# Optimization experiments

Hardware: AMD Instinct MI355X
Metric: run time of the kernel (lower is better)

The kernel has to match this reference:

```python
import jax, jax.numpy as jnp
import numpy as np

B, T, C, H = 2, 64, 384, 768
LR, MOM, DECAY = 0.01, 0.9, 0.001


def pscan(gates, tokens):
    """parallel_scan_log: x[t] = gates[t]*x[t-1] + tokens[t] along axis 1.
    gates [B,S], tokens [B,S,...]."""
    extra = tokens.ndim - gates.ndim
    g = gates.reshape(gates.shape + (1,) * extra)
    g = jnp.clip(g, 1e-7, 1.0 - 1e-7)
    lc = jnp.cumsum(jnp.log(g), axis=1)              # log cumulative gates
    return jnp.exp(lc) * jnp.cumsum(tokens * jnp.exp(-lc), axis=1)


def setup_inputs():
    key = jax.random.key(0)
    ks = jax.random.split(key, 12)
    s = 0.02
    W0 = jax.random.normal(ks[0], (H, C), jnp.float32) * s
    W1 = jax.random.normal(ks[1], (C, H), jnp.float32) * s
    return {
        "x": jax.random.normal(ks[2], (B, T, C), jnp.float32),
        "Wq": jax.random.normal(ks[3], (C, C), jnp.float32) * s, "bq": jnp.zeros((C,), jnp.float32),
        "Wk": jax.random.normal(ks[4], (C, C), jnp.float32) * s, "bk": jnp.zeros((C,), jnp.float32),
        "Wv": jax.random.normal(ks[5], (C, C), jnp.float32) * s, "bv": jnp.zeros((C,), jnp.float32),
        "Wo": jax.random.normal(ks[6], (C, C), jnp.float32) * s, "bo": jnp.zeros((C,), jnp.float32),
        "init_query": jax.random.normal(ks[7], (1, 1, C), jnp.float32) * s,
        "sW0": jnp.broadcast_to(W0, (B, H, C)) + 0.0,
        "sb0": jnp.zeros((B, H), jnp.float32),
        "sW1": jnp.broadcast_to(W1, (B, C, H)) + 0.0,
        "sb1": jnp.zeros((B, C), jnp.float32),
    }


def reference(x, Wq, bq, Wk, bk, Wv, bv, Wo, bo, init_query, sW0, sb0, sW1, sb1):
    dt = x.dtype
    # ---- retrieval (causal: uses init_query since no previous segment) ----
    q = jnp.broadcast_to(init_query, (B, 1, C)) @ Wq.T + bq          # [B,1,C]
    h_pre = jnp.einsum('bqc,bhc->bqh', q, sW0) + sb0[:, None]
    h = h_pre * jax.nn.sigmoid(h_pre)                                 # SiLU
    pred = jnp.einsum('bqh,bch->bqc', h, sW1) + sb1[:, None]
    out = pred @ Wo.T + bo                                            # [B,1,C]

    # ---- test-time memory update: per-token MSE gradients ----
    k = x @ Wk.T + bk                                                 # [B,T,C]
    v = x @ Wv.T + bv
    h1_pre = jnp.einsum('btc,bhc->bth', k, sW0) + sb0[:, None]
    sig = jax.nn.sigmoid(h1_pre)
    h1 = h1_pre * sig
    p = jnp.einsum('bth,bch->btc', h1, sW1) + sb1[:, None]
    dp = p - v                                                        # d(MSE)/d(pred)
    dW1 = jnp.einsum('btc,bth->btch', dp, h1)                         # [B,T,C,H]
    db1 = dp
    dh1 = jnp.einsum('btc,bch->bth', dp, sW1)
    dh1p = dh1 * (sig * (1 + h1_pre * (1 - sig)))                     # SiLU grad
    dW0 = jnp.einsum('bth,btc->bthc', dh1p, k)                        # [B,T,H,C]
    db0 = dh1p

    # ---- momentum scan + decayed weight scan ----
    def update(W, g):
        surprise = -LR * g                                            # [B,T,...]
        m = pscan(jnp.full((B, T), MOM, dt), (1.0 - MOM) * surprise)  # EMA of surprises
        toks = jnp.concatenate([W[:, None], m], axis=1)               # seed with current weight
        gts = jnp.concatenate([jnp.ones((B, 1), dt),
                               jnp.full((B, T), 1.0 - DECAY, dt)], axis=1)
        return pscan(gts, toks)[:, -1]                                # final weight after segment

    nW0 = update(sW0, dW0)
    nb0 = update(sb0, db0)
    nW1 = update(sW1, dW1)
    nb1 = update(sb1, db1)
    return out, nW0, nb0, nW1, nb1
```

## Files before the change

kernel.cpp:

```cpp
#include <hip/hip_runtime.h>
#include <hip/hip_bf16.h>
#include <cmath>

#define BB 2
#define TT 64
#define CC 384
#define HH 768

#define O_OUT 0
#define O_NW0 768
#define O_NB0 (768 + 589824)
#define O_NW1 (O_NB0 + 1536)
#define O_NB1 (O_NW1 + 589824)

struct Coefs { float ct[TT]; float dfac; };

typedef __attribute__((ext_vector_type(8))) short bf16x8;
typedef __attribute__((ext_vector_type(4))) float f32x4;

__device__ __forceinline__ float bf2f(unsigned short u) {
    union { unsigned int i; float f; } x; x.i = ((unsigned int)u) << 16; return x.f;
}
__device__ __forceinline__ unsigned short f2bf(float f) {
    union { float f; unsigned int i; } u; u.f = f;
    unsigned int x = u.i;
    unsigned int r = (x + 0x7fffu + ((x >> 16) & 1u)) >> 16;
    return (unsigned short)r;
}
__device__ __forceinline__ f32x4 mfma16(bf16x8 a, bf16x8 b, f32x4 c) {
    return __builtin_amdgcn_mfma_f32_16x16x32_bf16(a, b, c, 0, 0, 0);
}
__device__ __forceinline__ bf16x8 ldbf8(const unsigned short* p) {
    return *(const bf16x8*)p;
}
__device__ __forceinline__ bf16x8 ldcvt8(const float* p) {
    float4 a = *(const float4*)p, b = *(const float4*)(p + 4);
    bf16x8 r;
    r[0] = (short)f2bf(a.x); r[1] = (short)f2bf(a.y); r[2] = (short)f2bf(a.z); r[3] = (short)f2bf(a.w);
    r[4] = (short)f2bf(b.x); r[5] = (short)f2bf(b.y); r[6] = (short)f2bf(b.z); r[7] = (short)f2bf(b.w);
    return r;
}
__device__ __forceinline__ bf16x8 ldcvt8s(const float* p, int stride) {
    bf16x8 r;
    #pragma unroll
    for (int i = 0; i < 8; ++i) r[i] = (short)f2bf(p[(size_t)i * stride]);
    return r;
}

__global__ void __launch_bounds__(256) k_qkv(
        const float* __restrict__ x,
        const float* __restrict__ Wk, const float* __restrict__ bk,
        const float* __restrict__ Wv, const float* __restrict__ bv,
        const float* __restrict__ Wq, const float* __restrict__ bq,
        const float* __restrict__ iq,
        unsigned short* __restrict__ kb_bf, float* __restrict__ vb,
        float* __restrict__ qb) {
    const int blk = blockIdx.x, j = threadIdx.x;
    const int wid = j >> 6, L = j & 63;
    const int w = blk * 4 + wid;
    const int lrow = L & 15, kq = (L >> 4) * 8, quad = L >> 4;
    int mf, npair;
    if (w < 192) { mf = w % 8; npair = w / 8; }
    else         { mf = 8;     npair = 24 + (w - 192); }
    const float* Arow = (mf < 8) ? (x + (size_t)(mf * 16 + lrow) * CC) : iq;
    const int n0 = npair * 32 + lrow, n1 = n0 + 16;
    const float* B0 = (n0 < CC) ? (Wk + (size_t)n0 * CC)
                    : (n0 < 2 * CC) ? (Wv + (size_t)(n0 - CC) * CC)
                    : (Wq + (size_t)(n0 - 2 * CC) * CC);
    const float* B1 = (n1 < CC) ? (Wk + (size_t)n1 * CC)
                    : (n1 < 2 * CC) ? (Wv + (size_t)(n1 - CC) * CC)
                    : (Wq + (size_t)(n1 - 2 * CC) * CC);
    f32x4 acc0 = {0,0,0,0}, acc1 = {0,0,0,0};
    #pragma unroll 2
    for (int s = 0; s < CC / 32; ++s) {
        int k = s * 32 + kq;
        bf16x8 a = ldcvt8(Arow + k);
        bf16x8 b0 = ldcvt8(B0 + k), b1 = ldcvt8(B1 + k);
        acc0 = mfma16(a, b0, acc0); acc1 = mfma16(a, b1, acc1);
    }
    #pragma unroll
    for (int ni = 0; ni < 2; ++ni) {
        f32x4 acc = ni == 0 ? acc0 : acc1;
        int n = npair * 32 + ni * 16 + lrow;
        if (mf < 8) {
            #pragma unroll
            for (int r = 0; r < 4; ++r) {
                int m = mf * 16 + quad * 4 + r;
                float v = acc[r];
                if (n < CC) kb_bf[(size_t)m * CC + n] = f2bf(v + bk[n]);
                else        vb[(size_t)m * CC + (n - CC)] = v + bv[n - CC];
            }
        } else if (quad == 0) {
            qb[n - 2 * CC] = acc[0] + bq[n - 2 * CC];
        }
    }
}

__global__ void __launch_bounds__(256) k_h1(
        const unsigned short* __restrict__ kb_bf, const float* __restrict__ qb,
        const float* __restrict__ sW0, const float* __restrict__ sb0,
        unsigned short* __restrict__ h1_bf, float* __restrict__ dsil,
        float* __restrict__ hret) {
    const int blk = blockIdx.x, j = threadIdx.x;
    const int b = blk / 30;
    const int wid = j >> 6, L = j & 63;
    const int w = (blk % 30) * 4 + wid;
    const int mf = w % 5, npair = w / 5;
    const int lrow = L & 15, kq = (L >> 4) * 8, quad = L >> 4;
    const unsigned short* Abf = kb_bf + (size_t)(b * TT + mf * 16 + lrow) * CC;
    const int n0 = npair * 32 + lrow;
    const float* B0 = sW0 + (size_t)(b * HH + n0) * CC;
    const float* B1 = B0 + 16 * CC;
    f32x4 acc0 = {0,0,0,0}, acc1 = {0,0,0,0};
    if (mf < 4) {
        #pragma unroll 2
        for (int s = 0; s < CC / 32; ++s) {
            int k = s * 32 + kq;
            bf16x8 a = ldbf8(Abf + k);
            bf16x8 b0 = ldcvt8(B0 + k), b1 = ldcvt8(B1 + k);
            acc0 = mfma16(a, b0, acc0); acc1 = mfma16(a, b1, acc1);
        }
    } else {
        #pragma unroll 2
        for (int s = 0; s < CC / 32; ++s) {
            int k = s * 32 + kq;
            bf16x8 a = ldcvt8(qb + k);
            bf16x8 b0 = ldcvt8(B0 + k), b1 = ldcvt8(B1 + k);
            acc0 = mfma16(a, b0, acc0); acc1 = mfma16(a, b1, acc1);
        }
    }
    #pragma unroll
    for (int ni = 0; ni < 2; ++ni) {
        f32x4 acc = ni == 0 ? acc0 : acc1;
        int n = npair * 32 + ni * 16 + lrow;
        float bias = sb0[b * HH + n];
        if (mf < 4) {
            #pragma unroll
            for (int r = 0; r < 4; ++r) {
                int t = mf * 16 + quad * 4 + r;
                float pre = acc[r] + bias;
                float sig = 1.f / (1.f + expf(-pre));
                size_t idx = (size_t)(b * TT + t) * HH + n;
                h1_bf[idx] = f2bf(pre * sig);
                dsil[idx]  = sig * (1.f + pre * (1.f - sig));
            }
        } else if (quad == 0) {
            float pre = acc[0] + bias;
            float sig = 1.f / (1.f + expf(-pre));
            hret[b * HH + n] = pre * sig;
        }
    }
}

__global__ void __launch_bounds__(256) k_p(
        const unsigned short* __restrict__ h1_bf, const float* __restrict__ hret,
        const float* __restrict__ vb,
        const float* __restrict__ sW1, const float* __restrict__ sb1,
        unsigned short* __restrict__ dp_bf, float* __restrict__ pred) {
    const int blk = blockIdx.x, j = threadIdx.x;
    const int b = blk / 15;
    const int wid = j >> 6, L = j & 63;
    const int w = (blk % 15) * 4 + wid;
    const int mf = w % 5, npair = w / 5;
    const int lrow = L & 15, kq = (L >> 4) * 8, quad = L >> 4;
    const unsigned short* Abf = h1_bf + (size_t)(b * TT + mf * 16 + lrow) * HH;
    const float* Aq = hret + (size_t)b * HH;
    const int n0 = npair * 32 + lrow;
    const float* B0 = sW1 + (size_t)(b * CC + n0) * HH;
    const float* B1 = B0 + 16 * HH;
    f32x4 acc0 = {0,0,0,0}, acc1 = {0,0,0,0};
    if (mf < 4) {
        #pragma unroll 2
        for (int s = 0; s < HH / 32; ++s) {
            int k = s * 32 + kq;
            bf16x8 a = ldbf8(Abf + k);
            bf16x8 b0 = ldcvt8(B0 + k), b1 = ldcvt8(B1 + k);
            acc0 = mfma16(a, b0, acc0); acc1 = mfma16(a, b1, acc1);
        }
    } else {
        #pragma unroll 2
        for (int s = 0; s < HH / 32; ++s) {
            int k = s * 32 + kq;
            bf16x8 a = ldcvt8(Aq + k);
            bf16x8 b0 = ldcvt8(B0 + k), b1 = ldcvt8(B1 + k);
            acc0 = mfma16(a, b0, acc0); acc1 = mfma16(a, b1, acc1);
        }
    }
    #pragma unroll
    for (int ni = 0; ni < 2; ++ni) {
        f32x4 acc = ni == 0 ? acc0 : acc1;
        int n = npair * 32 + ni * 16 + lrow;
        float bias = sb1[b * CC + n];
        if (mf < 4) {
            #pragma unroll
            for (int r = 0; r < 4; ++r) {
                int t = mf * 16 + quad * 4 + r;
                size_t idx = (size_t)(b * TT + t) * CC + n;
                dp_bf[idx] = f2bf(acc[r] + bias - vb[idx]);
            }
        } else if (quad == 0) {
            pred[b * CC + n] = acc[0] + bias;
        }
    }
}

__global__ void __launch_bounds__(256) k_epi1(
        const unsigned short* __restrict__ dp_bf,
        const unsigned short* __restrict__ h1_bf,
        const float* __restrict__ dsil,
        const float* __restrict__ sW1, const float* __restrict__ sb1,
        const float* __restrict__ pred,
        const float* __restrict__ Wo, const float* __restrict__ bo,
        unsigned short* __restrict__ dh1p_bf,
        float* __restrict__ out, Coefs cf) {
    __shared__ float smem[6144];
    const int blk = blockIdx.x, j = threadIdx.x;
    if (blk < 48) {
        const int b = blk / 24;
        const int wid = j >> 6, L = j & 63;
        const int w = (blk % 24) * 4 + wid;
        const int mf = w % 4, npair = w / 4;
        const int lrow = L & 15, kq = (L >> 4) * 8, quad = L >> 4;
        const unsigned short* Abf = dp_bf + (size_t)(b * TT + mf * 16 + lrow) * CC;
        const int n0 = npair * 32 + lrow, n1 = n0 + 16;
        const float* Bb = sW1 + (size_t)b * CC * HH;
        f32x4 acc0 = {0,0,0,0}, acc1 = {0,0,0,0};
        for (int s = 0; s < CC / 32; ++s) {
            int k = s * 32 + kq;
            bf16x8 a = ldbf8(Abf + k);
            bf16x8 b0 = ldcvt8s(Bb + (size_t)k * HH + n0, HH);
            bf16x8 b1 = ldcvt8s(Bb + (size_t)k * HH + n1, HH);
            acc0 = mfma16(a, b0, acc0); acc1 = mfma16(a, b1, acc1);
        }
        #pragma unroll
        for (int ni = 0; ni < 2; ++ni) {
            f32x4 acc = ni == 0 ? acc0 : acc1;
            int n = npair * 32 + ni * 16 + lrow;
            #pragma unroll
            for (int r = 0; r < 4; ++r) {
                int t = mf * 16 + quad * 4 + r;
                size_t idx = (size_t)(b * TT + t) * HH + n;
                dh1p_bf[idx] = f2bf(acc[r] * dsil[idx]);
            }
        }
    } else if (blk < 336) {
        float* a_t = smem;
        float* e_t = smem + 2048;
        const int u = blk - 48;
        const int b = u / 144, rem = u % 144;
        const int c0 = (rem / 12) * 32, h0 = (rem % 12) * 64;
        for (int i = j; i < TT * 32; i += 256) {
            int t = i >> 5, c = i & 31;
            a_t[t * 32 + c] = cf.ct[t] * bf2f(dp_bf[((size_t)(b * TT + t)) * CC + c0 + c]);
        }
        for (int i = j; i < TT * 64; i += 256) {
            int t = i >> 6, h = i & 63;
            e_t[t * 64 + h] = bf2f(h1_bf[((size_t)(b * TT + t)) * HH + h0 + h]);
        }
        __syncthreads();
        const int ci = j & 31, hb = (j >> 5) * 8;
        float acc[8] = {0, 0, 0, 0, 0, 0, 0, 0};
        for (int t = 0; t < TT; ++t) {
            float av = a_t[t * 32 + ci];
            #pragma unroll
            for (int m = 0; m < 8; ++m) acc[m] += av * e_t[t * 64 + hb + m];
        }
        const size_t idx = ((size_t)b * CC + c0 + ci) * HH + h0 + hb;
        const float4* w4 = (const float4*)(sW1 + idx);
        float4 wa = w4[0], wb = w4[1];
        float4 o0, o1;
        o0.x = cf.dfac * wa.x - acc[0]; o0.y = cf.dfac * wa.y - acc[1];
        o0.z = cf.dfac * wa.z - acc[2]; o0.w = cf.dfac * wa.w - acc[3];
        o1.x = cf.dfac * wb.x - acc[4]; o1.y = cf.dfac * wb.y - acc[5];
        o1.z = cf.dfac * wb.z - acc[6]; o1.w = cf.dfac * wb.w - acc[7];
        *(float4*)(out + O_NW1 + idx) = o0;
        *(float4*)(out + O_NW1 + idx + 4) = o1;
        if (h0 == 0 && j < 32) {
            float s = 0.f;
            for (int t = 0; t < TT; ++t) s += a_t[t * 32 + j];
            out[O_NB1 + b * CC + c0 + j] = cf.dfac * sb1[b * CC + c0 + j] - s;
        }
    } else {
        const int rb = blk - 336;
        const int b = rb / 24, nt = rb % 24;
        if (j < CC / 4) ((float4*)smem)[j] = ((const float4*)(pred + b * CC))[j];
        __syncthreads();
        const int nl = j & 15, ks = j >> 4;
        const int n = nt * 16 + nl;
        const float4* wr = (const float4*)(Wo + (size_t)n * CC + ks * 24);
        float s = 0.f;
        #pragma unroll
        for (int i = 0; i < 6; ++i) {
            float4 a = wr[i];
            const float* v = smem + ks * 24 + i * 4;
            s += a.x * v[0] + a.y * v[1] + a.z * v[2] + a.w * v[3];
        }
        smem[1024 + ks * 17 + nl] = s;
        __syncthreads();
        if (j < 16) {
            int n2 = nt * 16 + j;
            float acc = bo[n2];
            #pragma unroll
            for (int kk = 0; kk < 16; ++kk) acc += smem[1024 + kk * 17 + j];
            out[O_OUT + b * CC + n2] = acc;
        }
    }
}

__global__ void __launch_bounds__(256) k_epi2(
        const unsigned short* __restrict__ dh1p_bf,
        const unsigned short* __restrict__ kb_bf,
        const float* __restrict__ sW0, const float* __restrict__ sb0,
        float* __restrict__ out, Coefs cf) {
    __shared__ float smem[6144];
    float* a_t = smem;
    float* e_t = smem + 2048;
    const int blk = blockIdx.x, j = threadIdx.x;
    const int b = blk / 144, rem = blk % 144;
    const int h0 = (rem / 6) * 32, c0 = (rem % 6) * 64;
    for (int i = j; i < TT * 32; i += 256) {
        int t = i >> 5, h = i & 31;
        a_t[t * 32 + h] = cf.ct[t] * bf2f(dh1p_bf[((size_t)(b * TT + t)) * HH + h0 + h]);
    }
    for (int i = j; i < TT * 64; i += 256) {
        int t = i >> 6, c = i & 63;
        e_t[t * 64 + c] = bf2f(kb_bf[((size_t)(b * TT + t)) * CC + c0 + c]);
    }
    __syncthreads();
    const int hi = j & 31, cb = (j >> 5) * 8;
    float acc[8] = {0, 0, 0, 0, 0, 0, 0, 0};
    for (int t = 0; t < TT; ++t) {
        float av = a_t[t * 32 + hi];
        #pragma unroll
        for (int m = 0; m < 8; ++m) acc[m] += av * e_t[t * 64 + cb + m];
    }
    const size_t idx = ((size_t)b * HH + h0 + hi) * CC + c0 + cb;
    const float4* w4 = (const float4*)(sW0 + idx);
    float4 wa = w4[0], wb = w4[1];
    float4 o0, o1;
    o0.x = cf.dfac * wa.x - acc[0]; o0.y = cf.dfac * wa.y - acc[1];
    o0.z = cf.dfac * wa.z - acc[2]; o0.w = cf.dfac * wa.w - acc[3];
    o1.x = cf.dfac * wb.x - acc[4]; o1.y = cf.dfac * wb.y - acc[5];
    o1.z = cf.dfac * wb.z - acc[6]; o1.w = cf.dfac * wb.w - acc[7];
    *(float4*)(out + O_NW0 + idx) = o0;
    *(float4*)(out + O_NW0 + idx + 4) = o1;
    if (c0 == 0 && j < 32) {
        float s = 0.f;
        for (int t = 0; t < TT; ++t) s += a_t[t * 32 + j];
        out[O_NB0 + b * HH + h0 + j] = cf.dfac * sb0[b * HH + h0 + j] - s;
    }
}

extern "C" void kernel_launch(void* const* d_in, const int* in_sizes, int n_in,
                              void* d_out, int out_size, void* d_ws, size_t ws_size,
                              hipStream_t stream) {
    const float* x   = (const float*)d_in[0];
    const float* Wq  = (const float*)d_in[1];
    const float* bq  = (const float*)d_in[2];
    const float* Wk  = (const float*)d_in[3];
    const float* bk  = (const float*)d_in[4];
    const float* Wv  = (const float*)d_in[5];
    const float* bv  = (const float*)d_in[6];
    const float* Wo  = (const float*)d_in[7];
    const float* bo  = (const float*)d_in[8];
    const float* iq  = (const float*)d_in[9];
    const float* sW0 = (const float*)d_in[10];
    const float* sb0 = (const float*)d_in[11];
    const float* sW1 = (const float*)d_in[12];
    const float* sb1 = (const float*)d_in[13];

    float* fw = (float*)d_ws;
    float* qb   = fw;
    float* hret = qb + 384;
    float* pred = hret + 1536;
    float* vb   = pred + 768;
    float* dsil = vb + 49152;
    unsigned short* us = (unsigned short*)(dsil + 98304);
    unsigned short* kb_bf   = us;
    unsigned short* h1_bf   = kb_bf + 49152;
    unsigned short* dp_bf   = h1_bf + 98304;
    unsigned short* dh1p_bf = dp_bf + 49152;

    Coefs cf;
    const double mom = 0.9, decay = 1.0 - 0.001, lr = 0.01;
    for (int s = 0; s < TT; ++s) {
        double sum = 0.0;
        for (int t = s; t < TT; ++t) sum += pow(decay, (double)(TT - 1 - t)) * pow(mom, (double)(t - s));
        cf.ct[s] = (float)(lr * (1.0 - mom) * sum);
    }
    cf.dfac = (float)pow(decay, (double)TT);

    k_qkv <<<dim3(51),  dim3(256), 0, stream>>>(x, Wk, bk, Wv, bv, Wq, bq, iq, kb_bf, vb, qb);
    k_h1  <<<dim3(60),  dim3(256), 0, stream>>>(kb_bf, qb, sW0, sb0, h1_bf, dsil, hret);
    k_p   <<<dim3(30),  dim3(256), 0, stream>>>(h1_bf, hret, vb, sW1, sb1, dp_bf, pred);
    k_epi1<<<dim3(384), dim3(256), 0, stream>>>(dp_bf, h1_bf, dsil, sW1, sb1, pred, Wo, bo,
                                                dh1p_bf, (float*)d_out, cf);
    k_epi2<<<dim3(288), dim3(256), 0, stream>>>(dh1p_bf, kb_bf, sW0, sb0, (float*)d_out, cf);
}
```

Baseline: 142.0 us.

## Fuse dh1 GEMM into dW0 epilogue and prefetch weights into cache in qkv

Drops the separate k_epi1 dh1 GEMM and k_epi2 launch. Each dW0 block now recomputes its 32-column dh1p slice directly into shared memory with MFMA, which removes the dh1p_bf round trip and one kernel launch at the cost of recomputing the sW1 GEMM across six c0 tiles. It also adds 512 extra blocks to k_qkv that read sW0, sW1 and Wo and write dummy sums, so these weights are warm in L2/MALL for later kernels. The warming is cache priming that adds memory traffic in the first kernel and relies on cache residency.

After: 138.2 us. 2.7% less time.

```diff
diff --git a/kernel.cpp b/kernel.cpp
--- a/kernel.cpp
+++ b/kernel.cpp
@@ -53,9 +53,25 @@
         const float* __restrict__ Wv, const float* __restrict__ bv,
         const float* __restrict__ Wq, const float* __restrict__ bq,
         const float* __restrict__ iq,
+        const float* __restrict__ sW0, const float* __restrict__ sW1,
+        const float* __restrict__ Wo,
         unsigned short* __restrict__ kb_bf, float* __restrict__ vb,
-        float* __restrict__ qb) {
+        float* __restrict__ qb, float* __restrict__ warm_sink) {
     const int blk = blockIdx.x, j = threadIdx.x;
+    if (blk >= 51) {
+        int t = (blk - 51) * 256 + j;
+        float acc = 0.f;
+        for (int g = t; g < 184320; g += 512 * 256) {
+            const float4* src; int off;
+            if      (g < 73728)  { src = (const float4*)sW0; off = g; }
+            else if (g < 147456) { src = (const float4*)sW1; off = g - 73728; }
+            else                 { src = (const float4*)Wo;  off = g - 147456; }
+            float4 v = src[off];
+            acc += v.x + v.y + v.z + v.w;
+        }
+        warm_sink[t] = acc;
+        return;
+    }
     const int wid = j >> 6, L = j & 63;
     const int w = blk * 4 + wid;
     const int lrow = L & 15, kq = (L >> 4) * 8, quad = L >> 4;
@@ -204,50 +220,22 @@
     }
 }
 
-__global__ void __launch_bounds__(256) k_epi1(
+__global__ void __launch_bounds__(256) k_epi(
         const unsigned short* __restrict__ dp_bf,
         const unsigned short* __restrict__ h1_bf,
+        const unsigned short* __restrict__ kb_bf,
         const float* __restrict__ dsil,
+        const float* __restrict__ sW0, const float* __restrict__ sb0,
         const float* __restrict__ sW1, const float* __restrict__ sb1,
         const float* __restrict__ pred,
         const float* __restrict__ Wo, const float* __restrict__ bo,
-        unsigned short* __restrict__ dh1p_bf,
         float* __restrict__ out, Coefs cf) {
     __shared__ float smem[6144];
     const int blk = blockIdx.x, j = threadIdx.x;
-    if (blk < 48) {
-        const int b = blk / 24;
-        const int wid = j >> 6, L = j & 63;
-        const int w = (blk % 24) * 4 + wid;
-        const int mf = w % 4, npair = w / 4;
-        const int lrow = L & 15, kq = (L >> 4) * 8, quad = L >> 4;
-        const unsigned short* Abf = dp_bf + (size_t)(b * TT + mf * 16 + lrow) * CC;
-        const int n0 = npair * 32 + lrow, n1 = n0 + 16;
-        const float* Bb = sW1 + (size_t)b * CC * HH;
-        f32x4 acc0 = {0,0,0,0}, acc1 = {0,0,0,0};
-        for (int s = 0; s < CC / 32; ++s) {
-            int k = s * 32 + kq;
-            bf16x8 a = ldbf8(Abf + k);
-            bf16x8 b0 = ldcvt8s(Bb + (size_t)k * HH + n0, HH);
-            bf16x8 b1 = ldcvt8s(Bb + (size_t)k * HH + n1, HH);
-            acc0 = mfma16(a, b0, acc0); acc1 = mfma16(a, b1, acc1);
-        }
-        #pragma unroll
-        for (int ni = 0; ni < 2; ++ni) {
-            f32x4 acc = ni == 0 ? acc0 : acc1;
-            int n = npair * 32 + ni * 16 + lrow;
-            #pragma unroll
-            for (int r = 0; r < 4; ++r) {
-                int t = mf * 16 + quad * 4 + r;
-                size_t idx = (size_t)(b * TT + t) * HH + n;
-                dh1p_bf[idx] = f2bf(acc[r] * dsil[idx]);
-            }
-        }
-    } else if (blk < 336) {
+    if (blk < 288) {
         float* a_t = smem;
         float* e_t = smem + 2048;
-        const int u = blk - 48;
-        const int b = u / 144, rem = u % 144;
+        const int b = blk / 144, rem = blk % 144;
         const int c0 = (rem / 12) * 32, h0 = (rem % 12) * 64;
         for (int i = j; i < TT * 32; i += 256) {
             int t = i >> 5, c = i & 31;
@@ -280,8 +268,65 @@
             for (int t = 0; t < TT; ++t) s += a_t[t * 32 + j];
             out[O_NB1 + b * CC + c0 + j] = cf.dfac * sb1[b * CC + c0 + j] - s;
         }
+    } else if (blk < 576) {
+        float* a_t = smem;
+        float* e_t = smem + 2048;
+        const int u = blk - 288;
+        const int b = u / 144, rem = u % 144;
+        const int h0 = (rem / 6) * 32, c0 = (rem % 6) * 64;
+        for (int i = j; i < TT * 64; i += 256) {
+            int t = i >> 6, c = i & 63;
+            e_t[t * 64 + c] = bf2f(kb_bf[((size_t)(b * TT + t)) * CC + c0 + c]);
+        }
+        const int wid = j >> 6, L = j & 63;
+        const int lrow = L & 15, kq = (L >> 4) * 8, quad = L >> 4;
+        const unsigned short* Abf = dp_bf + (size_t)(b * TT + wid * 16 + lrow) * CC;
+        const float* Bb = sW1 + (size_t)b * CC * HH;
+        const int n0 = h0 + lrow, n1 = h0 + 16 + lrow;
+        f32x4 acc0 = {0,0,0,0}, acc1 = {0,0,0,0};
+        for (int s = 0; s < CC / 32; ++s) {
+            int k = s * 32 + kq;
+            bf16x8 a = ldbf8(Abf + k);
+            bf16x8 b0 = ldcvt8s(Bb + (size_t)k * HH + n0, HH);
+            bf16x8 b1 = ldcvt8s(Bb + (size_t)k * HH + n1, HH);
+            acc0 = mfma16(a, b0, acc0); acc1 = mfma16(a, b1, acc1);
+        }
+        #pragma unroll
+        for (int ni = 0; ni < 2; ++ni) {
+            f32x4 acc = ni == 0 ? acc0 : acc1;
+            int hl = ni * 16 + lrow;
+            #pragma unroll
+            for (int r = 0; r < 4; ++r) {
+                int t = wid * 16 + quad * 4 + r;
+                float ds = dsil[(size_t)(b * TT + t) * HH + h0 + hl];
+                a_t[t * 32 + hl] = cf.ct[t] * (acc[r] * ds);
+            }
+        }
+        __syncthreads();
+        const int hi = j & 31, cb = (j >> 5) * 8;
+        float acc[8] = {0, 0, 0, 0, 0, 0, 0, 0};
+        for (int t = 0; t < TT; ++t) {
+            float av = a_t[t * 32 + hi];
+            #pragma unroll
+            for (int m = 0; m < 8; ++m) acc[m] += av * e_t[t * 64 + cb + m];
+        }
+        const size_t idx = ((size_t)b * HH + h0 + hi) * CC + c0 + cb;
+        const float4* w4 = (const float4*)(sW0 + idx);
+        float4 wa = w4[0], wb = w4[1];
+        float4 o0, o1;
+        o0.x = cf.dfac * wa.x - acc[0]; o0.y = cf.dfac * wa.y - acc[1];
+        o0.z = cf.dfac * wa.z - acc[2]; o0.w = cf.dfac * wa.w - acc[3];
+        o1.x = cf.dfac * wb.x - acc[4]; o1.y = cf.dfac * wb.y - acc[5];
+        o1.z = cf.dfac * wb.z - acc[6]; o1.w = cf.dfac * wb.w - acc[7];
+        *(float4*)(out + O_NW0 + idx) = o0;
+        *(float4*)(out + O_NW0 + idx + 4) = o1;
+        if (c0 == 0 && j < 32) {
+            float s = 0.f;
+            for (int t = 0; t < TT; ++t) s += a_t[t * 32 + j];
+            out[O_NB0 + b * HH + h0 + j] = cf.dfac * sb0[b * HH + h0 + j] - s;
+        }
     } else {
-        const int rb = blk - 336;
+        const int rb = blk - 576;
         const int b = rb / 24, nt = rb % 24;
         if (j < CC / 4) ((float4*)smem)[j] = ((const float4*)(pred + b * CC))[j];
         __syncthreads();
@@ -304,50 +349,6 @@
             for (int kk = 0; kk < 16; ++kk) acc += smem[1024 + kk * 17 + j];
             out[O_OUT + b * CC + n2] = acc;
         }
-    }
-}
-
-__global__ void __launch_bounds__(256) k_epi2(
-        const unsigned short* __restrict__ dh1p_bf,
-        const unsigned short* __restrict__ kb_bf,
-        const float* __restrict__ sW0, const float* __restrict__ sb0,
-        float* __restrict__ out, Coefs cf) {
-    __shared__ float smem[6144];
-    float* a_t = smem;
-    float* e_t = smem + 2048;
-    const int blk = blockIdx.x, j = threadIdx.x;
-    const int b = blk / 144, rem = blk % 144;
-    const int h0 = (rem / 6) * 32, c0 = (rem % 6) * 64;
-    for (int i = j; i < TT * 32; i += 256) {
-        int t = i >> 5, h = i & 31;
-        a_t[t * 32 + h] = cf.ct[t] * bf2f(dh1p_bf[((size_t)(b * TT + t)) * HH + h0 + h]);
-    }
-    for (int i = j; i < TT * 64; i += 256) {
-        int t = i >> 6, c = i & 63;
-        e_t[t * 64 + c] = bf2f(kb_bf[((size_t)(b * TT + t)) * CC + c0 + c]);
-    }
-    __syncthreads();
-    const int hi = j & 31, cb = (j >> 5) * 8;
-    float acc[8] = {0, 0, 0, 0, 0, 0, 0, 0};
-    for (int t = 0; t < TT; ++t) {
-        float av = a_t[t * 32 + hi];
-        #pragma unroll
-        for (int m = 0; m < 8; ++m) acc[m] += av * e_t[t * 64 + cb + m];
-    }
-    const size_t idx = ((size_t)b * HH + h0 + hi) * CC + c0 + cb;
-    const float4* w4 = (const float4*)(sW0 + idx);
-    float4 wa = w4[0], wb = w4[1];
-    float4 o0, o1;
-    o0.x = cf.dfac * wa.x - acc[0]; o0.y = cf.dfac * wa.y - acc[1];
-    o0.z = cf.dfac * wa.z - acc[2]; o0.w = cf.dfac * wa.w - acc[3];
-    o1.x = cf.dfac * wb.x - acc[4]; o1.y = cf.dfac * wb.y - acc[5];
-    o1.z = cf.dfac * wb.z - acc[6]; o1.w = cf.dfac * wb.w - acc[7];
-    *(float4*)(out + O_NW0 + idx) = o0;
-    *(float4*)(out + O_NW0 + idx + 4) = o1;
-    if (c0 == 0 && j < 32) {
-        float s = 0.f;
-        for (int t = 0; t < TT; ++t) s += a_t[t * 32 + j];
-        out[O_NB0 + b * HH + h0 + j] = cf.dfac * sb0[b * HH + h0 + j] - s;
     }
 }
 
@@ -375,11 +376,11 @@
     float* pred = hret + 1536;
     float* vb   = pred + 768;
     float* dsil = vb + 49152;
-    unsigned short* us = (unsigned short*)(dsil + 98304);
-    unsigned short* kb_bf   = us;
-    unsigned short* h1_bf   = kb_bf + 49152;
-    unsigned short* dp_bf   = h1_bf + 98304;
-    unsigned short* dh1p_bf = dp_bf + 49152;
+    float* warm = dsil + 98304;
+    unsigned short* us = (unsigned short*)(warm + 131072);
+    unsigned short* kb_bf = us;
+    unsigned short* h1_bf = kb_bf + 49152;
+    unsigned short* dp_bf = h1_bf + 98304;
 
     Coefs cf;
     const double mom = 0.9, decay = 1.0 - 0.001, lr = 0.01;
@@ -390,10 +391,10 @@
     }
     cf.dfac = (float)pow(decay, (double)TT);
 
-    k_qkv <<<dim3(51),  dim3(256), 0, stream>>>(x, Wk, bk, Wv, bv, Wq, bq, iq, kb_bf, vb, qb);
-    k_h1  <<<dim3(60),  dim3(256), 0, stream>>>(kb_bf, qb, sW0, sb0, h1_bf, dsil, hret);
-    k_p   <<<dim3(30),  dim3(256), 0, stream>>>(h1_bf, hret, vb, sW1, sb1, dp_bf, pred);
-    k_epi1<<<dim3(384), dim3(256), 0, stream>>>(dp_bf, h1_bf, dsil, sW1, sb1, pred, Wo, bo,
-                                                dh1p_bf, (float*)d_out, cf);
-    k_epi2<<<dim3(288), dim3(256), 0, stream>>>(dh1p_bf, kb_bf, sW0, sb0, (float*)d_out, cf);
-}
+    k_qkv<<<dim3(563), dim3(256), 0, stream>>>(x, Wk, bk, Wv, bv, Wq, bq, iq, sW0, sW1, Wo,
+                                               kb_bf, vb, qb, warm);
+    k_h1 <<<dim3(60),  dim3(256), 0, stream>>>(kb_bf, qb, sW0, sb0, h1_bf, dsil, hret);
+    k_p  <<<dim3(30),  dim3(256), 0, stream>>>(h1_bf, hret, vb, sW1, sb1, dp_bf, pred);
+    k_epi<<<dim3(624), dim3(256), 0, stream>>>(dp_bf, h1_bf, kb_bf, dsil, sW0, sb0, sW1, sb1,
+                                               pred, Wo, bo, (float*)d_out, cf);
+}
```
